# Kernel tuning notes

Measured on AMD Instinct MI355X. Metric: run time of the kernel, lower is better.

## Reference

```python
import jax, jax.numpy as jnp
import numpy as np

DT = 0.02          # full control timestep (cfg dt)
N_SUBSTEPS = 8     # RK4 substeps per forward call
LMBDA = 0.5        # first-order actuator lag gain
G_VEC = jnp.array([0.0, 0.0, -9.81], dtype=jnp.float32)
N_ENVS = 2097152


def setup_inputs() -> dict:
    key = jax.random.key(0)
    k1, k2 = jax.random.split(key)
    X0 = jax.random.normal(k1, (N_ENVS, 9), dtype=jnp.float32)
    U = jax.random.normal(k2, (N_ENVS, 3), dtype=jnp.float32)
    return {"X0": X0, "U": U}


def reference(X0, U):
    h = DT / N_SUBSTEPS  # substep size

    def dynamics(X):
        v = X[:, 3:6]
        a = X[:, 6:9]
        a_dot = LMBDA * (U - a) / DT   # actuator lag uses full dt, as in torch code
        # X_dot = [p_dot, v_dot, a_dot] = [v, a - g_vec, a_dot]
        return jnp.concatenate([v, a - G_VEC, a_dot], axis=-1)

    def rk4_step(X, _):
        k1 = dynamics(X)
        k2 = dynamics(X + 0.5 * h * k1)
        k3 = dynamics(X + 0.5 * h * k2)
        k4 = dynamics(X + h * k3)
        X_next = X + (h / 6.0) * (k1 + 2.0 * k2 + 2.0 * k3 + k4)
        return X_next, None

    X_final, _ = jax.lax.scan(rk4_step, X0, None, length=N_SUBSTEPS)
    return X_final
```

## Files before the change

kernel.cpp:

```cpp
#include <hip/hip_runtime.h>


#define THREADS 256

struct Coeffs {
    float P00, P01, P02;
    float P10, P11, P12;
    float P20, P21, P22;
    float Ku0, Ku1, Ku2;
    float G0,  G1,  G2;
};

__global__ __launch_bounds__(THREADS)
void pointmass_kernel(const float* __restrict__ X0,
                      const float* __restrict__ U,
                      float* __restrict__ Out,
                      int envTotal, Coeffs cf) {
    const int tid = blockIdx.x * THREADS + threadIdx.x;
    const int envBase = tid * 4;
    if (envBase >= envTotal) return;

    if (envBase + 4 <= envTotal) {
        const float4* x4 = (const float4*)(X0 + (size_t)envBase * 9);
        const float4* u4 = (const float4*)(U  + (size_t)envBase * 3);
        float4*       o4 = (float4*)(Out + (size_t)envBase * 9);

        float4 xin[9], uin[3], oo[9];
        #pragma unroll
        for (int j = 0; j < 9; ++j) xin[j] = x4[j];
        #pragma unroll
        for (int j = 0; j < 3; ++j) uin[j] = u4[j];

        const float* x = (const float*)xin;
        const float* u = (const float*)uin;
        float*       o = (float*)oo;

        #pragma unroll
        for (int m = 0; m < 4; ++m) {
            #pragma unroll
            for (int k = 0; k < 3; ++k) {
                const float p  = x[9 * m + k];
                const float v  = x[9 * m + 3 + k];
                const float a  = x[9 * m + 6 + k];
                const float uu = u[3 * m + k];
                float r0 = cf.P00 * p + cf.P01 * v + cf.P02 * a + cf.Ku0 * uu;
                float r1 = cf.P10 * p + cf.P11 * v + cf.P12 * a + cf.Ku1 * uu;
                float r2 = cf.P20 * p + cf.P21 * v + cf.P22 * a + cf.Ku2 * uu;
                if (k == 2) { r0 += cf.G0; r1 += cf.G1; r2 += cf.G2; }
                o[9 * m + k]     = r0;
                o[9 * m + 3 + k] = r1;
                o[9 * m + 6 + k] = r2;
            }
        }

        #pragma unroll
        for (int j = 0; j < 9; ++j) o4[j] = oo[j];
    } else {
        for (int e = envBase; e < envTotal; ++e) {
            float p[3], v[3], a[3], uu[3];
            for (int k = 0; k < 3; ++k) {
                p[k]  = X0[(size_t)e * 9 + k];
                v[k]  = X0[(size_t)e * 9 + 3 + k];
                a[k]  = X0[(size_t)e * 9 + 6 + k];
                uu[k] = U[(size_t)e * 3 + k];
            }
            for (int k = 0; k < 3; ++k) {
                float r0 = cf.P00 * p[k] + cf.P01 * v[k] + cf.P02 * a[k] + cf.Ku0 * uu[k];
                float r1 = cf.P10 * p[k] + cf.P11 * v[k] + cf.P12 * a[k] + cf.Ku1 * uu[k];
                float r2 = cf.P20 * p[k] + cf.P21 * v[k] + cf.P22 * a[k] + cf.Ku2 * uu[k];
                if (k == 2) { r0 += cf.G0; r1 += cf.G1; r2 += cf.G2; }
                Out[(size_t)e * 9 + k]     = r0;
                Out[(size_t)e * 9 + 3 + k] = r1;
                Out[(size_t)e * 9 + 6 + k] = r2;
            }
        }
    }
}

static void mat3_mul(const double A[3][3], const double B[3][3], double C[3][3]) {
    for (int i = 0; i < 3; ++i)
        for (int j = 0; j < 3; ++j) {
            double s = 0.0;
            for (int k = 0; k < 3; ++k) s += A[i][k] * B[k][j];
            C[i][j] = s;
        }
}
static void mat3_copy(const double A[3][3], double B[3][3]) {
    for (int i = 0; i < 3; ++i) for (int j = 0; j < 3; ++j) B[i][j] = A[i][j];
}

extern "C" void kernel_launch(void* const* d_in, const int* in_sizes, int n_in,
                              void* d_out, int out_size, void* d_ws, size_t ws_size,
                              hipStream_t stream) {
    const float* X0 = (const float*)d_in[0];
    const float* U  = (const float*)d_in[1];
    float* Out = (float*)d_out;
    const int envTotal = in_sizes[0] / 9;

    const double DT = 0.02;
    const double h = DT / 8.0;
    const double c = 0.5 / DT;
    double hA[3][3] = {{0, h, 0}, {0, 0, h}, {0, 0, -c * h}};

    double hA2[3][3], hA3[3][3], hA4[3][3];
    mat3_mul(hA, hA, hA2);
    mat3_mul(hA2, hA, hA3);
    mat3_mul(hA3, hA, hA4);

    double P[3][3], Q[3][3];
    for (int i = 0; i < 3; ++i)
        for (int j = 0; j < 3; ++j) {
            const double I = (i == j) ? 1.0 : 0.0;
            P[i][j] = I + hA[i][j] + hA2[i][j] / 2.0 + hA3[i][j] / 6.0 + hA4[i][j] / 24.0;
            Q[i][j] = h * (I + hA[i][j] / 2.0 + hA2[i][j] / 6.0 + hA3[i][j] / 24.0);
        }

    double P2[3][3], P4[3][3], P8[3][3];
    mat3_mul(P, P, P2);
    mat3_mul(P2, P2, P4);
    mat3_mul(P4, P4, P8);

    double IP[3][3], IP2[3][3], IP4[3][3], T[3][3], S[3][3], R[3][3];
    mat3_copy(P, IP);  mat3_copy(P2, IP2);  mat3_copy(P4, IP4);
    for (int i = 0; i < 3; ++i) { IP[i][i] += 1.0; IP2[i][i] += 1.0; IP4[i][i] += 1.0; }
    mat3_mul(IP, IP2, T);
    mat3_mul(T, IP4, S);
    mat3_mul(S, Q, R);

    Coeffs cf;
    cf.P00 = (float)P8[0][0]; cf.P01 = (float)P8[0][1]; cf.P02 = (float)P8[0][2];
    cf.P10 = (float)P8[1][0]; cf.P11 = (float)P8[1][1]; cf.P12 = (float)P8[1][2];
    cf.P20 = (float)P8[2][0]; cf.P21 = (float)P8[2][1]; cf.P22 = (float)P8[2][2];
    cf.Ku0 = (float)(R[0][2] * c); cf.Ku1 = (float)(R[1][2] * c); cf.Ku2 = (float)(R[2][2] * c);
    cf.G0 = (float)(R[0][1] * 9.81);
    cf.G1 = (float)(R[1][1] * 9.81);
    cf.G2 = (float)(R[2][1] * 9.81);

    const int nThreads = (envTotal + 3) / 4;
    const int blocks = (nThreads + THREADS - 1) / THREADS;
    pointmass_kernel<<<blocks, THREADS, 0, stream>>>(X0, U, Out, envTotal, cf);
}
```

Baseline: 180.1 us.

## Stage tiles through double-buffered LDS with coalesced loads in persistent blocks

Replaces the per-thread strided float4 loads (each thread reading 36 contiguous floats) with a persistent grid of 1536 blocks. Each block loads contiguous 256-environment tiles with fully coalesced float4 accesses, stages them in double-buffered shared memory, and prefetches the next tile into registers while computing the current one. Outputs are computed per element from LDS and written as coalesced float4 stores. This adds per-element integer div/mod, LDS traffic and a barrier per tile, and the single barrier per iteration with double buffering could be racy if a buffer is reused before all reads finish.

```diff
diff --git a/kernel.cpp b/kernel.cpp
--- a/kernel.cpp
+++ b/kernel.cpp
@@ -2,6 +2,11 @@
 
 
 #define THREADS 256
+#define TILE_ENVS 256
+#define TILE_XF   (TILE_ENVS * 9)
+#define TILE_UF   (TILE_ENVS * 3)
+#define TILE_X4   (TILE_XF / 4)
+#define TILE_U4   (TILE_UF / 4)
 
 struct Coeffs {
     float P00, P01, P02;
@@ -11,68 +16,124 @@
     float G0,  G1,  G2;
 };
 
+__device__ __forceinline__ float compute_elem(const float* __restrict__ sx,
+                                              const float* __restrict__ su,
+                                              int gi, const Coeffs& cf) {
+    const int e = (unsigned)gi / 9u;
+    const int c = gi - 9 * e;
+    const int r = (unsigned)c / 3u;
+    const int k = c - 3 * r;
+    const float p = sx[e * 9 + k];
+    const float v = sx[e * 9 + 3 + k];
+    const float a = sx[e * 9 + 6 + k];
+    const float u = su[e * 3 + k];
+    const float A  = (r == 0) ? cf.P00 : ((r == 1) ? cf.P10 : cf.P20);
+    const float B  = (r == 0) ? cf.P01 : ((r == 1) ? cf.P11 : cf.P21);
+    const float C  = (r == 0) ? cf.P02 : ((r == 1) ? cf.P12 : cf.P22);
+    const float Ku = (r == 0) ? cf.Ku0 : ((r == 1) ? cf.Ku1 : cf.Ku2);
+    const float Gr = (r == 0) ? cf.G0  : ((r == 1) ? cf.G1  : cf.G2);
+    float res = A * p + B * v + C * a + Ku * u;
+    if (k == 2) res += Gr;
+    return res;
+}
+
 __global__ __launch_bounds__(THREADS)
 void pointmass_kernel(const float* __restrict__ X0,
                       const float* __restrict__ U,
                       float* __restrict__ Out,
-                      int envTotal, Coeffs cf) {
-    const int tid = blockIdx.x * THREADS + threadIdx.x;
-    const int envBase = tid * 4;
-    if (envBase >= envTotal) return;
-
-    if (envBase + 4 <= envTotal) {
-        const float4* x4 = (const float4*)(X0 + (size_t)envBase * 9);
-        const float4* u4 = (const float4*)(U  + (size_t)envBase * 3);
-        float4*       o4 = (float4*)(Out + (size_t)envBase * 9);
-
-        float4 xin[9], uin[3], oo[9];
-        #pragma unroll
-        for (int j = 0; j < 9; ++j) xin[j] = x4[j];
-        #pragma unroll
-        for (int j = 0; j < 3; ++j) uin[j] = u4[j];
-
-        const float* x = (const float*)xin;
-        const float* u = (const float*)uin;
-        float*       o = (float*)oo;
-
-        #pragma unroll
-        for (int m = 0; m < 4; ++m) {
-            #pragma unroll
-            for (int k = 0; k < 3; ++k) {
-                const float p  = x[9 * m + k];
-                const float v  = x[9 * m + 3 + k];
-                const float a  = x[9 * m + 6 + k];
-                const float uu = u[3 * m + k];
-                float r0 = cf.P00 * p + cf.P01 * v + cf.P02 * a + cf.Ku0 * uu;
-                float r1 = cf.P10 * p + cf.P11 * v + cf.P12 * a + cf.Ku1 * uu;
-                float r2 = cf.P20 * p + cf.P21 * v + cf.P22 * a + cf.Ku2 * uu;
-                if (k == 2) { r0 += cf.G0; r1 += cf.G1; r2 += cf.G2; }
-                o[9 * m + k]     = r0;
-                o[9 * m + 3 + k] = r1;
-                o[9 * m + 6 + k] = r2;
-            }
-        }
-
-        #pragma unroll
-        for (int j = 0; j < 9; ++j) o4[j] = oo[j];
-    } else {
-        for (int e = envBase; e < envTotal; ++e) {
-            float p[3], v[3], a[3], uu[3];
-            for (int k = 0; k < 3; ++k) {
-                p[k]  = X0[(size_t)e * 9 + k];
-                v[k]  = X0[(size_t)e * 9 + 3 + k];
-                a[k]  = X0[(size_t)e * 9 + 6 + k];
-                uu[k] = U[(size_t)e * 3 + k];
-            }
-            for (int k = 0; k < 3; ++k) {
-                float r0 = cf.P00 * p[k] + cf.P01 * v[k] + cf.P02 * a[k] + cf.Ku0 * uu[k];
-                float r1 = cf.P10 * p[k] + cf.P11 * v[k] + cf.P12 * a[k] + cf.Ku1 * uu[k];
-                float r2 = cf.P20 * p[k] + cf.P21 * v[k] + cf.P22 * a[k] + cf.Ku2 * uu[k];
-                if (k == 2) { r0 += cf.G0; r1 += cf.G1; r2 += cf.G2; }
-                Out[(size_t)e * 9 + k]     = r0;
-                Out[(size_t)e * 9 + 3 + k] = r1;
-                Out[(size_t)e * 9 + 6 + k] = r2;
-            }
+                      int envTotal, int numTiles, Coeffs cf) {
+    __shared__ float sX[2][TILE_XF];
+    __shared__ float sU[2][TILE_UF];
+
+    const int t = threadIdx.x;
+    const int stride = gridDim.x;
+
+    int tile = blockIdx.x;
+    float4 rx0, rx1, rx2, ru0;
+    {
+        const float4* gx = (const float4*)(X0 + (size_t)tile * TILE_XF);
+        const float4* gu = (const float4*)(U  + (size_t)tile * TILE_UF);
+        rx0 = gx[t];
+        rx1 = gx[t + 256];
+        if (t < TILE_X4 - 512) rx2 = gx[t + 512];
+        if (t < TILE_U4)       ru0 = gu[t];
+    }
+
+    int buf = 0;
+    for (; tile < numTiles; tile += stride) {
+        float4* lx = (float4*)sX[buf];
+        float4* lu = (float4*)sU[buf];
+        lx[t]       = rx0;
+        lx[t + 256] = rx1;
+        if (t < TILE_X4 - 512) lx[t + 512] = rx2;
+        if (t < TILE_U4)       lu[t]       = ru0;
+
+        __syncthreads();
+
+        const int nt = tile + stride;
+        if (nt < numTiles) {
+            const float4* gx = (const float4*)(X0 + (size_t)nt * TILE_XF);
+            const float4* gu = (const float4*)(U  + (size_t)nt * TILE_UF);
+            rx0 = gx[t];
+            rx1 = gx[t + 256];
+            if (t < TILE_X4 - 512) rx2 = gx[t + 512];
+            if (t < TILE_U4)       ru0 = gu[t];
+        }
+
+        const float* sx = sX[buf];
+        const float* su = sU[buf];
+        float4* o4 = (float4*)(Out + (size_t)tile * TILE_XF);
+
+        {
+            const int s = t;
+            float4 o;
+            o.x = compute_elem(sx, su, 4 * s + 0, cf);
+            o.y = compute_elem(sx, su, 4 * s + 1, cf);
+            o.z = compute_elem(sx, su, 4 * s + 2, cf);
+            o.w = compute_elem(sx, su, 4 * s + 3, cf);
+            o4[s] = o;
+        }
+        {
+            const int s = t + 256;
+            float4 o;
+            o.x = compute_elem(sx, su, 4 * s + 0, cf);
+            o.y = compute_elem(sx, su, 4 * s + 1, cf);
+            o.z = compute_elem(sx, su, 4 * s + 2, cf);
+            o.w = compute_elem(sx, su, 4 * s + 3, cf);
+            o4[s] = o;
+        }
+        if (t < TILE_X4 - 512) {
+            const int s = t + 512;
+            float4 o;
+            o.x = compute_elem(sx, su, 4 * s + 0, cf);
+            o.y = compute_elem(sx, su, 4 * s + 1, cf);
+            o.z = compute_elem(sx, su, 4 * s + 2, cf);
+            o.w = compute_elem(sx, su, 4 * s + 3, cf);
+            o4[s] = o;
+        }
+
+        buf ^= 1;
+    }
+
+    const int remBase = numTiles * TILE_ENVS;
+    const int rem = envTotal - remBase;
+    if (rem > 0 && blockIdx.x == 0 && t < rem) {
+        const int e = remBase + t;
+        float p[3], v[3], a[3], uu[3];
+        for (int k = 0; k < 3; ++k) {
+            p[k]  = X0[(size_t)e * 9 + k];
+            v[k]  = X0[(size_t)e * 9 + 3 + k];
+            a[k]  = X0[(size_t)e * 9 + 6 + k];
+            uu[k] = U[(size_t)e * 3 + k];
+        }
+        for (int k = 0; k < 3; ++k) {
+            float r0 = cf.P00 * p[k] + cf.P01 * v[k] + cf.P02 * a[k] + cf.Ku0 * uu[k];
+            float r1 = cf.P10 * p[k] + cf.P11 * v[k] + cf.P12 * a[k] + cf.Ku1 * uu[k];
+            float r2 = cf.P20 * p[k] + cf.P21 * v[k] + cf.P22 * a[k] + cf.Ku2 * uu[k];
+            if (k == 2) { r0 += cf.G0; r1 += cf.G1; r2 += cf.G2; }
+            Out[(size_t)e * 9 + k]     = r0;
+            Out[(size_t)e * 9 + 3 + k] = r1;
+            Out[(size_t)e * 9 + 6 + k] = r2;
         }
     }
 }
@@ -136,7 +197,7 @@
     cf.G1 = (float)(R[1][1] * 9.81);
     cf.G2 = (float)(R[2][1] * 9.81);
 
-    const int nThreads = (envTotal + 3) / 4;
-    const int blocks = (nThreads + THREADS - 1) / THREADS;
-    pointmass_kernel<<<blocks, THREADS, 0, stream>>>(X0, U, Out, envTotal, cf);
-}
+    const int numTiles = envTotal / TILE_ENVS;
+    int blocks = numTiles < 1536 ? (numTiles > 0 ? numTiles : 1) : 1536;
+    pointmass_kernel<<<blocks, THREADS, 0, stream>>>(X0, U, Out, envTotal, numTiles, cf);
+}
```

New measurement: 166.3 us. 7.6% less time.

## Remap threads so each lane handles one env axis with contiguous stores

Applied to the files above, without the earlier changes.

Reorganizes work so each 64-lane wave processes chunks of 21 environments, with each lane computing one axis (row r) of one env and writing three contiguous floats. Stores become contiguous across lanes, and each lane does fewer loads per chunk, replacing the previous one-thread-four-envs float4 scheme. The cost is that 1 of 64 lanes sits idle per chunk, loads are 12-byte unaligned reads duplicated across three lanes (served by cache), and each wave loops over four chunks.

```diff
diff --git a/kernel.cpp b/kernel.cpp
--- a/kernel.cpp
+++ b/kernel.cpp
@@ -2,6 +2,8 @@
 
 
 #define THREADS 256
+#define CHUNK_ENVS 21
+#define CHUNKS_PER_WAVE 4
 
 struct Coeffs {
     float P00, P01, P02;
@@ -11,68 +13,47 @@
     float G0,  G1,  G2;
 };
 
+struct F3 { float x, y, z; };
+
 __global__ __launch_bounds__(THREADS)
 void pointmass_kernel(const float* __restrict__ X0,
                       const float* __restrict__ U,
                       float* __restrict__ Out,
-                      int envTotal, Coeffs cf) {
-    const int tid = blockIdx.x * THREADS + threadIdx.x;
-    const int envBase = tid * 4;
-    if (envBase >= envTotal) return;
+                      int envTotal, int chunksTotal, Coeffs cf) {
+    const int tid  = blockIdx.x * THREADS + threadIdx.x;
+    const int wave = tid >> 6;
+    const int lane = tid & 63;
+    const int r = lane % 3;
+    const int m = lane / 3;
 
-    if (envBase + 4 <= envTotal) {
-        const float4* x4 = (const float4*)(X0 + (size_t)envBase * 9);
-        const float4* u4 = (const float4*)(U  + (size_t)envBase * 3);
-        float4*       o4 = (float4*)(Out + (size_t)envBase * 9);
+    const float A  = (r == 0) ? cf.P00 : ((r == 1) ? cf.P10 : cf.P20);
+    const float B  = (r == 0) ? cf.P01 : ((r == 1) ? cf.P11 : cf.P21);
+    const float C  = (r == 0) ? cf.P02 : ((r == 1) ? cf.P12 : cf.P22);
+    const float Ku = (r == 0) ? cf.Ku0 : ((r == 1) ? cf.Ku1 : cf.Ku2);
+    const float G  = (r == 0) ? cf.G0  : ((r == 1) ? cf.G1  : cf.G2);
 
-        float4 xin[9], uin[3], oo[9];
-        #pragma unroll
-        for (int j = 0; j < 9; ++j) xin[j] = x4[j];
-        #pragma unroll
-        for (int j = 0; j < 3; ++j) uin[j] = u4[j];
+    const int chunk0 = wave * CHUNKS_PER_WAVE;
 
-        const float* x = (const float*)xin;
-        const float* u = (const float*)uin;
-        float*       o = (float*)oo;
+    #pragma unroll
+    for (int j = 0; j < CHUNKS_PER_WAVE; ++j) {
+        const int chunk = chunk0 + j;
+        if (chunk >= chunksTotal) break;
+        const int envBase = chunk * CHUNK_ENVS;
+        const int remEnvs = envTotal - envBase;
+        const int actEnvs = remEnvs < CHUNK_ENVS ? remEnvs : CHUNK_ENVS;
+        if (lane < 3 * actEnvs) {
+            const size_t xoff = (size_t)envBase * 9 + 9 * m;
+            const F3 p = *(const F3*)(X0 + xoff);
+            const F3 v = *(const F3*)(X0 + xoff + 3);
+            const F3 a = *(const F3*)(X0 + xoff + 6);
+            const F3 u = *(const F3*)(U + (size_t)(envBase + m) * 3);
 
-        #pragma unroll
-        for (int m = 0; m < 4; ++m) {
-            #pragma unroll
-            for (int k = 0; k < 3; ++k) {
-                const float p  = x[9 * m + k];
-                const float v  = x[9 * m + 3 + k];
-                const float a  = x[9 * m + 6 + k];
-                const float uu = u[3 * m + k];
-                float r0 = cf.P00 * p + cf.P01 * v + cf.P02 * a + cf.Ku0 * uu;
-                float r1 = cf.P10 * p + cf.P11 * v + cf.P12 * a + cf.Ku1 * uu;
-                float r2 = cf.P20 * p + cf.P21 * v + cf.P22 * a + cf.Ku2 * uu;
-                if (k == 2) { r0 += cf.G0; r1 += cf.G1; r2 += cf.G2; }
-                o[9 * m + k]     = r0;
-                o[9 * m + 3 + k] = r1;
-                o[9 * m + 6 + k] = r2;
-            }
-        }
+            F3 o;
+            o.x = A * p.x + B * v.x + C * a.x + Ku * u.x;
+            o.y = A * p.y + B * v.y + C * a.y + Ku * u.y;
+            o.z = A * p.z + B * v.z + C * a.z + Ku * u.z + G;
 
-        #pragma unroll
-        for (int j = 0; j < 9; ++j) o4[j] = oo[j];
-    } else {
-        for (int e = envBase; e < envTotal; ++e) {
-            float p[3], v[3], a[3], uu[3];
-            for (int k = 0; k < 3; ++k) {
-                p[k]  = X0[(size_t)e * 9 + k];
-                v[k]  = X0[(size_t)e * 9 + 3 + k];
-                a[k]  = X0[(size_t)e * 9 + 6 + k];
-                uu[k] = U[(size_t)e * 3 + k];
-            }
-            for (int k = 0; k < 3; ++k) {
-                float r0 = cf.P00 * p[k] + cf.P01 * v[k] + cf.P02 * a[k] + cf.Ku0 * uu[k];
-                float r1 = cf.P10 * p[k] + cf.P11 * v[k] + cf.P12 * a[k] + cf.Ku1 * uu[k];
-                float r2 = cf.P20 * p[k] + cf.P21 * v[k] + cf.P22 * a[k] + cf.Ku2 * uu[k];
-                if (k == 2) { r0 += cf.G0; r1 += cf.G1; r2 += cf.G2; }
-                Out[(size_t)e * 9 + k]     = r0;
-                Out[(size_t)e * 9 + 3 + k] = r1;
-                Out[(size_t)e * 9 + 6 + k] = r2;
-            }
+            *(F3*)(Out + (size_t)envBase * 9 + 3 * lane) = o;
         }
     }
 }
@@ -136,7 +117,8 @@
     cf.G1 = (float)(R[1][1] * 9.81);
     cf.G2 = (float)(R[2][1] * 9.81);
 
-    const int nThreads = (envTotal + 3) / 4;
-    const int blocks = (nThreads + THREADS - 1) / THREADS;
-    pointmass_kernel<<<blocks, THREADS, 0, stream>>>(X0, U, Out, envTotal, cf);
+    const int chunksTotal = (envTotal + CHUNK_ENVS - 1) / CHUNK_ENVS;
+    const int wavesNeeded = (chunksTotal + CHUNKS_PER_WAVE - 1) / CHUNKS_PER_WAVE;
+    const int blocks = (wavesNeeded + (THREADS / 64) - 1) / (THREADS / 64);
+    pointmass_kernel<<<blocks, THREADS, 0, stream>>>(X0, U, Out, envTotal, chunksTotal, cf);
 }
```

Measured after the change: 156.0 us. 1.15x faster.
